# Kernel tuning notes

Measured on AMD Instinct MI355X. Metric: run time of the kernel, lower is better.

Reference implementation:

```python
import jax, jax.numpy as jnp
import numpy as np

ATTN, ENC, DEC = 1024, 1024, 1024
B, S = 64, 2048

def setup_inputs() -> dict:
    key = jax.random.key(0)
    k1, k2, k3, k4, k5, k6 = jax.random.split(key, 6)
    sc_w = 1.0 / np.sqrt(ENC + DEC)
    sc_v = 1.0 / np.sqrt(ATTN)
    return {
        "hidden": jax.random.normal(k1, (B, DEC), dtype=jnp.float32),
        "vectors_to_attend": jax.random.normal(k2, (S, B, ENC), dtype=jnp.float32),
        "attn_w_weight": jax.random.uniform(k3, (ATTN, ENC + DEC), jnp.float32, -sc_w, sc_w),
        "attn_w_bias": jax.random.uniform(k4, (ATTN,), jnp.float32, -sc_w, sc_w),
        "attn_v_weight": jax.random.uniform(k5, (1, ATTN), jnp.float32, -sc_v, sc_v),
        "attn_v_bias": jax.random.uniform(k6, (1,), jnp.float32, -sc_v, sc_v),
    }

def reference(hidden, vectors_to_attend, attn_w_weight, attn_w_bias, attn_v_weight, attn_v_bias):
    # vectors_to_attend: [S, B, E] -> [B, S, E]
    v = jnp.transpose(vectors_to_attend, (1, 0, 2))
    # Split attn_w over the concat dim: concat([v, h]) @ W^T == v @ We^T + h @ Wd^T
    We = attn_w_weight[:, :ENC]   # [A, E]
    Wd = attn_w_weight[:, ENC:]   # [A, D]
    # energies: [B, S, A]
    e = jnp.tanh(jnp.einsum('bse,ae->bsa', v, We)
                 + jnp.einsum('bd,ad->ba', hidden, Wd)[:, None, :]
                 + attn_w_bias)
    # scores: [B, S]
    scores = jnp.einsum('bsa,a->bs', e, attn_v_weight[0]) + attn_v_bias[0]
    weights = jax.nn.softmax(scores, axis=1)          # softmax over seq dim
    context = jnp.einsum('bs,bse->be', weights, v)    # [B, E]
    return context[:, None, :]                        # [B, 1, E] to match bmm output
```

## Files before the change

kernel.cpp:

```cpp
#include <hip/hip_runtime.h>
#include <hip/hip_bf16.h>
#include <math.h>

#define BB 64
#define SS 2048
#define MT (SS*BB)
#define NT 16

typedef __attribute__((ext_vector_type(4))) float f4;
typedef __attribute__((ext_vector_type(8))) short s8;

__device__ __forceinline__ unsigned short f2bf(float x) {
  union { float f; unsigned u; } v; v.f = x;
  unsigned r = v.u + 0x7FFFu + ((v.u >> 16) & 1u);
  return (unsigned short)(r >> 16);
}
__device__ __forceinline__ float bf2f(unsigned short x) {
  union { unsigned u; float f; } v; v.u = ((unsigned)x) << 16;
  return v.f;
}
__device__ __forceinline__ float fast_tanh(float x) {
  float t = __expf(2.0f * x);
  return 1.0f - 2.0f * __builtin_amdgcn_rcpf(t + 1.0f);
}

#define GLD16(gp, lp) __builtin_amdgcn_global_load_lds( \
    (const __attribute__((address_space(1))) void*)(gp), \
    (__attribute__((address_space(3))) void*)(lp), 16, 0, 0)
#define WAITV4() asm volatile("s_waitcnt vmcnt(4)" ::: "memory")
#define WAITV0() asm volatile("s_waitcnt vmcnt(0)" ::: "memory")
#define BAR()    __builtin_amdgcn_s_barrier()
#define SCHED0() __builtin_amdgcn_sched_barrier(0)

__global__ void k_pack(const float* __restrict__ src, unsigned short* __restrict__ dst,
                       int stride) {
  __shared__ float ls[64][260];
  int g = blockIdx.x, cb = blockIdx.y, tid = threadIdx.x;
  int cl = (tid & 63) * 4, rbk = tid >> 6;
  const float* s0 = src + (size_t)(g * 64) * stride + cb * 256 + cl;
  #pragma unroll
  for (int it = 0; it < 16; ++it) {
    int rr = it * 4 + rbk;
    *(f4*)&ls[rr][cl] = *(const f4*)(s0 + (size_t)rr * stride);
  }
  __syncthreads();
  int kt_l = tid >> 6;
  int rr = tid & 63;
  int kt = cb * 4 + kt_l;
  int grow = g * 64 + rr;
  int panel = grow >> 8, pr = grow & 255, h = pr >> 7, r = pr & 127;
  unsigned short* d = dst + (((size_t)panel * 16 + kt) * 2 + h) * 8192 + r * 64;
  int rx = r & 7;
  #pragma unroll
  for (int sp = 0; sp < 8; ++sp) {
    const float* q = &ls[rr][kt_l * 64 + ((sp ^ rx) * 8)];
    f4 x0 = *(const f4*)q, x1 = *(const f4*)(q + 4);
    s8 o;
    #pragma unroll
    for (int j = 0; j < 4; ++j) { o[j] = (short)f2bf(x0[j]); o[4 + j] = (short)f2bf(x1[j]); }
    *(s8*)(d + sp * 8) = o;
  }
}

__global__ void k_hp(const float* __restrict__ hidden, const float* __restrict__ w,
                     const float* __restrict__ wbias, float* __restrict__ hp) {
  __shared__ float hs[1024];
  int b = blockIdx.x, tid = threadIdx.x;
  for (int i = tid; i < 1024; i += 256) hs[i] = hidden[b * 1024 + i];
  __syncthreads();
  int a = blockIdx.y * 256 + tid;
  const f4* wd = (const f4*)(w + a * 2048 + 1024);
  const f4* hv = (const f4*)hs;
  float acc = wbias[a];
  #pragma unroll 8
  for (int d = 0; d < 256; ++d) {
    f4 x = wd[d], y = hv[d];
    acc += x[0]*y[0] + x[1]*y[1] + x[2]*y[2] + x[3]*y[3];
  }
  hp[b * 1024 + a] = acc;
}

__global__ __launch_bounds__(512, 1) void k_gemm(
    const unsigned short* __restrict__ Avbs, const unsigned short* __restrict__ Wbs,
    const float* __restrict__ hp, const float* __restrict__ vw,
    float* __restrict__ part, int bm0, int nbm) {
  extern __shared__ char smem[];
  int bid = blockIdx.x;
  int nwg = nbm * 4;
  int wg = bid;
  if ((nwg & 7) == 0) { int cpx = nwg >> 3; wg = (bid & 7) * cpx + (bid >> 3); }
  int bn = wg & 3;
  int bmL = wg >> 2;
  int tid = threadIdx.x, lane = tid & 63;
  int wid = tid >> 6, wr = wid >> 2, wc = wid & 3;
  int c = lane & 15, kq = lane >> 4;

  int sx0 = ((kq) ^ (c & 7)) << 4;
  int sx1 = ((4 + kq) ^ (c & 7)) << 4;
  int aoff = wr * 16384 + c * 128;
  int boff = 32768 + (wc >> 1) * 16384 + ((wc & 1) * 64 + c) * 128;

  const unsigned short* Abase = Avbs + (size_t)bmL * 262144 + tid * 8;
  const unsigned short* Bbase = Wbs + (size_t)bn * 262144 + tid * 8;
  auto stage = [&](int tt, int u) {
    char* d = smem + (tt & 1) * 65536 + u * 16384 + tid * 16;
    const unsigned short* s = ((u & 2) ? Bbase : Abase) + ((size_t)tt * 2 + (u & 1)) * 8192;
    GLD16(s, d);
    GLD16(s + 4096, d + 8192);
  };

  f4 acc[8][4];
  f4 z = {0.f, 0.f, 0.f, 0.f};
  #pragma unroll
  for (int i = 0; i < 8; ++i)
    #pragma unroll
    for (int j = 0; j < 4; ++j) acc[i][j] = z;

  s8 vaC[4], vaN[4], vb0[4], vb1[4];

#define LDSA(DST, BASE, SX) { const char* p_ = (BASE) + (SX); \
    DST[0] = *(const s8*)(p_);        DST[1] = *(const s8*)(p_ + 2048); \
    DST[2] = *(const s8*)(p_ + 4096); DST[3] = *(const s8*)(p_ + 6144); }
#define LDB(RB, DST, SX) { const char* bb_ = (RB) + boff + (SX); \
    DST[0] = *(const s8*)(bb_);        DST[1] = *(const s8*)(bb_ + 2048); \
    DST[2] = *(const s8*)(bb_ + 4096); DST[3] = *(const s8*)(bb_ + 6144); }
#define MM(mh, VA, VB) { \
    __builtin_amdgcn_s_setprio(1); \
    _Pragma("unroll") \
    for (int m_ = 0; m_ < 4; ++m_) { \
      acc[(mh)*4+m_][0] = __builtin_amdgcn_mfma_f32_16x16x32_bf16(VA[m_], VB[0], acc[(mh)*4+m_][0], 0, 0, 0); \
      acc[(mh)*4+m_][1] = __builtin_amdgcn_mfma_f32_16x16x32_bf16(VA[m_], VB[1], acc[(mh)*4+m_][1], 0, 0, 0); \
      acc[(mh)*4+m_][2] = __builtin_amdgcn_mfma_f32_16x16x32_bf16(VA[m_], VB[2], acc[(mh)*4+m_][2], 0, 0, 0); \
      acc[(mh)*4+m_][3] = __builtin_amdgcn_mfma_f32_16x16x32_bf16(VA[m_], VB[3], acc[(mh)*4+m_][3], 0, 0, 0); \
    } \
    __builtin_amdgcn_s_setprio(0); }

  stage(0, 0); stage(0, 1); stage(0, 2); stage(0, 3);
  stage(1, 2); stage(1, 3);
  WAITV4();
  BAR();
  SCHED0();
  {
    const char* rb = smem;
    LDSA(vaC, rb + aoff, sx0);
    LDB(rb, vb0, sx0);
  }

  #pragma unroll 1
  for (int t = 0; t < NT; ++t) {
    const char* rb = smem + (t & 1) * 65536;
    const char* ab = rb + aoff;
    if (t < 15) stage(t + 1, 0);
    MM(0, vaC, vb0);
    LDSA(vaN, ab, sx1);
    LDB(rb, vb1, sx1);
    if (t < 15) stage(t + 1, 1);
    MM(0, vaN, vb1);
    LDSA(vaC, ab + 8192, sx0);
    SCHED0();
    BAR();
    SCHED0();
    if (t < 14) stage(t + 2, 2);
    MM(1, vaC, vb0);
    LDSA(vaN, ab + 8192, sx1);
    if (t < 14) stage(t + 2, 3);
    MM(1, vaN, vb1);
    if (t < 15) {
      if (t < 14) WAITV4(); else WAITV0();
      SCHED0();
      BAR();
      SCHED0();
      const char* nrb = smem + ((t + 1) & 1) * 65536;
      LDSA(vaC, nrb + aoff, sx0);
      LDB(nrb, vb0, sx0);
    }
  }
#undef LDSA
#undef LDB
#undef MM

  __syncthreads();
  {
    const float* hprow = hp + bn * 256;
    float* lhp = (float*)smem;
    #pragma unroll
    for (int qd = 0; qd < 8; ++qd) {
      int i = qd * 512 + tid;
      int b = i >> 6, col4 = i & 63;
      *(f4*)(lhp + b * 256 + col4 * 4) = *(const f4*)(hprow + (size_t)b * 1024 + col4 * 4);
    }
  }
  __syncthreads();
  const float* lhpf = (const float*)smem;

  int lg = kq;
  int bm = bm0 + bmL;
  float rs[8][4];
  #pragma unroll
  for (int mi = 0; mi < 8; ++mi)
    #pragma unroll
    for (int j = 0; j < 4; ++j) rs[mi][j] = 0.f;
  #pragma unroll
  for (int ni = 0; ni < 4; ++ni) {
    int colL = wc * 64 + ni * 16 + c;
    float vwa = vw[bn * 256 + colL];
    #pragma unroll
    for (int mi = 0; mi < 8; ++mi) {
      #pragma unroll
      for (int j = 0; j < 4; ++j) {
        int r = wr * 128 + mi * 16 + lg * 4 + j;
        int b = r & 63;
        float x = acc[mi][ni][j] + lhpf[b * 256 + colL];
        rs[mi][j] += fast_tanh(x) * vwa;
      }
    }
  }
  #pragma unroll
  for (int off = 1; off < 16; off <<= 1) {
    #pragma unroll
    for (int mi = 0; mi < 8; ++mi)
      #pragma unroll
      for (int j = 0; j < 4; ++j)
        rs[mi][j] += __shfl_xor(rs[mi][j], off, 64);
  }
  if (c == 0) {
    int p = bn * 4 + wc;
    #pragma unroll
    for (int mi = 0; mi < 8; ++mi)
      #pragma unroll
      for (int j = 0; j < 4; ++j) {
        int m = bm * 256 + wr * 128 + mi * 16 + lg * 4 + j;
        int b = m & 63, s = m >> 6;
        part[(size_t)p * MT + b * SS + s] = rs[mi][j];
      }
  }
}

__global__ void k_softmax(const float* __restrict__ part, float* __restrict__ wt) {
  int b = blockIdx.x, tid = threadIdx.x, lane = tid & 63, wid = tid >> 6;
  __shared__ float red[8];
  float sc[8];
  float mx = -1e30f;
  #pragma unroll
  for (int i = 0; i < 8; ++i) {
    int s = tid + i * 256;
    float a = 0.f;
    #pragma unroll
    for (int p = 0; p < 16; ++p) a += part[(size_t)p * MT + b * SS + s];
    sc[i] = a; mx = fmaxf(mx, a);
  }
  for (int o = 1; o < 64; o <<= 1) mx = fmaxf(mx, __shfl_xor(mx, o, 64));
  if (lane == 0) red[wid] = mx;
  __syncthreads();
  mx = fmaxf(fmaxf(red[0], red[1]), fmaxf(red[2], red[3]));
  float sum = 0.f;
  #pragma unroll
  for (int i = 0; i < 8; ++i) { sc[i] = expf(sc[i] - mx); sum += sc[i]; }
  for (int o = 1; o < 64; o <<= 1) sum += __shfl_xor(sum, o, 64);
  if (lane == 0) red[4 + wid] = sum;
  __syncthreads();
  sum = red[4] + red[5] + red[6] + red[7];
  float inv = 1.f / sum;
  #pragma unroll
  for (int i = 0; i < 8; ++i) wt[b * SS + tid + i * 256] = sc[i] * inv;
}

__global__ void k_ctx_bfs(const unsigned short* __restrict__ vbs, const float* __restrict__ wt,
                          float* __restrict__ ctxp) {
  int b = blockIdx.x, cch = blockIdx.y, tid = threadIdx.x;
  int e = tid * 4;
  int kt = e >> 6, sl = (e >> 3) & 7, off = e & 7;
  f4 acc = {0.f, 0.f, 0.f, 0.f};
  int s0 = cch * 128;
  const float* wrow = wt + b * SS;
  #pragma unroll 4
  for (int s = s0; s < s0 + 128; ++s) {
    float ws = wrow[s];
    int row = s * 64 + b;
    int panel = row >> 8, pr = row & 255, h = pr >> 7, r = pr & 127;
    size_t addr = (((size_t)panel * 16 + kt) * 2 + h) * 8192 + r * 64 + ((sl ^ (r & 7)) << 3) + off;
    ushort4 u = *(const ushort4*)(vbs + addr);
    acc[0] += bf2f(u.x) * ws;
    acc[1] += bf2f(u.y) * ws;
    acc[2] += bf2f(u.z) * ws;
    acc[3] += bf2f(u.w) * ws;
  }
  *(f4*)(ctxp + (size_t)(cch * 64 + b) * 1024 + tid * 4) = acc;
}

__global__ void k_ctx_f32(const float* __restrict__ v, const float* __restrict__ wt,
                          float* __restrict__ ctxp) {
  int b = blockIdx.x, cch = blockIdx.y, tid = threadIdx.x;
  f4 acc = {0.f, 0.f, 0.f, 0.f};
  int s0 = cch * 128;
  const float* wrow = wt + b * SS;
  #pragma unroll 4
  for (int s = s0; s < s0 + 128; ++s) {
    float ws = wrow[s];
    const f4* vp = (const f4*)(v + (size_t)(s * 64 + b) * 1024);
    acc += vp[tid] * ws;
  }
  *(f4*)(ctxp + (size_t)(cch * 64 + b) * 1024 + tid * 4) = acc;
}

__global__ void k_out(const float* __restrict__ ctxp, float* __restrict__ out) {
  int b = blockIdx.x, tid = threadIdx.x;
  f4 acc = {0.f, 0.f, 0.f, 0.f};
  #pragma unroll
  for (int cch = 0; cch < 16; ++cch)
    acc += *(const f4*)(ctxp + (size_t)(cch * 64 + b) * 1024 + tid * 4);
  *(f4*)(out + b * 1024 + tid * 4) = acc;
}

extern "C" void kernel_launch(void* const* d_in, const int* in_sizes, int n_in,
                              void* d_out, int out_size, void* d_ws, size_t ws_size,
                              hipStream_t stream) {
  const float* hidden = (const float*)d_in[0];
  const float* v      = (const float*)d_in[1];
  const float* ww     = (const float*)d_in[2];
  const float* wbias  = (const float*)d_in[3];
  const float* vwgt   = (const float*)d_in[4];
  float* out = (float*)d_out;

  char* ws = (char*)d_ws;
  float*          hp   = (float*)(ws);
  unsigned short* wbs  = (unsigned short*)(ws + 262144);
  float*          part = (float*)(ws + 262144 + 2097152);
  float*          wt   = (float*)(ws + 262144 + 2097152 + 8388608);
  float*          ctxp = (float*)(ws + 262144 + 2097152 + 8388608 + 524288);
  size_t fixed = 262144 + 2097152 + 8388608 + 524288 + 4194304;
  unsigned short* vbs  = (unsigned short*)(ws + fixed);

  size_t avail = (ws_size > fixed) ? (ws_size - fixed) : 0;
  long rows_chunk = (long)(avail / 2048) & ~511L;
  if (rows_chunk > MT) rows_chunk = MT;
  if (rows_chunk < 512) rows_chunk = 512;
  int nchunks = (int)((MT + rows_chunk - 1) / rows_chunk);

  hipFuncSetAttribute((const void*)k_gemm, hipFuncAttributeMaxDynamicSharedMemorySize, 131072);

  k_pack<<<dim3(16, 4), 256, 0, stream>>>(ww, wbs, 2048);
  k_hp<<<dim3(64, 4), 256, 0, stream>>>(hidden, ww, wbias, hp);

  for (long r0 = 0; r0 < MT; r0 += rows_chunk) {
    long nr = MT - r0; if (nr > rows_chunk) nr = rows_chunk;
    int nbm = (int)(nr / 256);
    k_pack<<<dim3((int)(nr / 64), 4), 256, 0, stream>>>(v + (size_t)r0 * 1024, vbs, 1024);
    k_gemm<<<nbm * 4, 512, 131072, stream>>>(vbs, wbs, hp, vwgt, part, (int)(r0 / 256), nbm);
  }

  k_softmax<<<64, 256, 0, stream>>>(part, wt);
  if (nchunks == 1)
    k_ctx_bfs<<<dim3(64, 16), 256, 0, stream>>>(vbs, wt, ctxp);
  else
    k_ctx_f32<<<dim3(64, 16), 256, 0, stream>>>(v, wt, ctxp);
  k_out<<<64, 256, 0, stream>>>(ctxp, out);
}
```

Before: 576.4 us.

## Quantize energy GEMM operands to FP8 and use scaled f8f6f4 MFMA

The packing kernel now converts the attended vectors and the attention weight to FP8 instead of bf16. The GEMM uses the 16x16x128 scaled f8f6f4 MFMA with unit scales, which halves the K iterations and halves the bytes packed and staged through LDS. Because the packed FP8 copy is too lossy for the context sum, the context kernel always reads the original fp32 vectors. This trades extra fp32 traffic in that pass, and accuracy of the energies and softmax scores, for lower GEMM compute and memory traffic.

```diff
diff --git a/kernel.cpp b/kernel.cpp
--- a/kernel.cpp
+++ b/kernel.cpp
@@ -5,20 +5,12 @@
 #define BB 64
 #define SS 2048
 #define MT (SS*BB)
-#define NT 16
+#define NT 8
 
 typedef __attribute__((ext_vector_type(4))) float f4;
-typedef __attribute__((ext_vector_type(8))) short s8;
-
-__device__ __forceinline__ unsigned short f2bf(float x) {
-  union { float f; unsigned u; } v; v.f = x;
-  unsigned r = v.u + 0x7FFFu + ((v.u >> 16) & 1u);
-  return (unsigned short)(r >> 16);
-}
-__device__ __forceinline__ float bf2f(unsigned short x) {
-  union { unsigned u; float f; } v; v.u = ((unsigned)x) << 16;
-  return v.f;
-}
+typedef __attribute__((ext_vector_type(4))) int   i4;
+typedef __attribute__((ext_vector_type(8))) int   i8;
+
 __device__ __forceinline__ float fast_tanh(float x) {
   float t = __expf(2.0f * x);
   return 1.0f - 2.0f * __builtin_amdgcn_rcpf(t + 1.0f);
@@ -32,8 +24,8 @@
 #define BAR()    __builtin_amdgcn_s_barrier()
 #define SCHED0() __builtin_amdgcn_sched_barrier(0)
 
-__global__ void k_pack(const float* __restrict__ src, unsigned short* __restrict__ dst,
-                       int stride) {
+__global__ void k_packq(const float* __restrict__ src, unsigned char* __restrict__ dst,
+                        int stride) {
   __shared__ float ls[64][260];
   int g = blockIdx.x, cb = blockIdx.y, tid = threadIdx.x;
   int cl = (tid & 63) * 4, rbk = tid >> 6;
@@ -44,21 +36,27 @@
     *(f4*)&ls[rr][cl] = *(const f4*)(s0 + (size_t)rr * stride);
   }
   __syncthreads();
-  int kt_l = tid >> 6;
   int rr = tid & 63;
-  int kt = cb * 4 + kt_l;
+  int q = tid >> 6;
+  int kt = cb * 2 + (q >> 1);
   int grow = g * 64 + rr;
   int panel = grow >> 8, pr = grow & 255, h = pr >> 7, r = pr & 127;
-  unsigned short* d = dst + (((size_t)panel * 16 + kt) * 2 + h) * 8192 + r * 64;
   int rx = r & 7;
-  #pragma unroll
-  for (int sp = 0; sp < 8; ++sp) {
-    const float* q = &ls[rr][kt_l * 64 + ((sp ^ rx) * 8)];
-    f4 x0 = *(const f4*)q, x1 = *(const f4*)(q + 4);
-    s8 o;
-    #pragma unroll
-    for (int j = 0; j < 4; ++j) { o[j] = (short)f2bf(x0[j]); o[4 + j] = (short)f2bf(x1[j]); }
-    *(s8*)(d + sp * 8) = o;
+  unsigned char* ub = dst + (((size_t)(panel * 8 + kt) * 2 + h) * 128 + r) * 128;
+  #pragma unroll
+  for (int si = 0; si < 4; ++si) {
+    int s = (q & 1) * 4 + si;
+    int sp = s ^ rx;
+    const float* fp = &ls[rr][q * 64 + si * 16];
+    i4 w;
+    #pragma unroll
+    for (int k = 0; k < 4; ++k) {
+      int b = 0;
+      b = __builtin_amdgcn_cvt_pk_fp8_f32(fp[k * 4 + 0], fp[k * 4 + 1], b, 0);
+      b = __builtin_amdgcn_cvt_pk_fp8_f32(fp[k * 4 + 2], fp[k * 4 + 3], b, 1);
+      w[k] = b;
+    }
+    *(i4*)(ub + sp * 16) = w;
   }
 }
 
@@ -80,8 +78,15 @@
   hp[b * 1024 + a] = acc;
 }
 
+__device__ __forceinline__ i8 build8(i4 lo, i4 hi) {
+  i8 r;
+  r[0] = lo[0]; r[1] = lo[1]; r[2] = lo[2]; r[3] = lo[3];
+  r[4] = hi[0]; r[5] = hi[1]; r[6] = hi[2]; r[7] = hi[3];
+  return r;
+}
+
 __global__ __launch_bounds__(512, 1) void k_gemm(
-    const unsigned short* __restrict__ Avbs, const unsigned short* __restrict__ Wbs,
+    const unsigned char* __restrict__ Aq, const unsigned char* __restrict__ Wq,
     const float* __restrict__ hp, const float* __restrict__ vw,
     float* __restrict__ part, int bm0, int nbm) {
   extern __shared__ char smem[];
@@ -95,18 +100,18 @@
   int wid = tid >> 6, wr = wid >> 2, wc = wid & 3;
   int c = lane & 15, kq = lane >> 4;
 
-  int sx0 = ((kq) ^ (c & 7)) << 4;
-  int sx1 = ((4 + kq) ^ (c & 7)) << 4;
-  int aoff = wr * 16384 + c * 128;
-  int boff = 32768 + (wc >> 1) * 16384 + ((wc & 1) * 64 + c) * 128;
-
-  const unsigned short* Abase = Avbs + (size_t)bmL * 262144 + tid * 8;
-  const unsigned short* Bbase = Wbs + (size_t)bn * 262144 + tid * 8;
+  int sx0 = ((2 * kq) ^ (c & 7)) << 4;
+  int sx1 = sx0 ^ 16;
+  int aoff0 = wr * 16384 + c * 128;
+  int boff0 = 32768 + (wc >> 1) * 16384 + ((wc & 1) * 64 + c) * 128;
+
+  const unsigned char* Abase = Aq + (size_t)bmL * 262144 + tid * 16;
+  const unsigned char* Bbase = Wq + (size_t)bn * 262144 + tid * 16;
   auto stage = [&](int tt, int u) {
     char* d = smem + (tt & 1) * 65536 + u * 16384 + tid * 16;
-    const unsigned short* s = ((u & 2) ? Bbase : Abase) + ((size_t)tt * 2 + (u & 1)) * 8192;
+    const unsigned char* s = ((u & 2) ? Bbase : Abase) + ((size_t)tt * 2 + (u & 1)) * 16384;
     GLD16(s, d);
-    GLD16(s + 4096, d + 8192);
+    GLD16(s + 8192, d + 8192);
   };
 
   f4 acc[8][4];
@@ -116,22 +121,28 @@
     #pragma unroll
     for (int j = 0; j < 4; ++j) acc[i][j] = z;
 
-  s8 vaC[4], vaN[4], vb0[4], vb1[4];
-
-#define LDSA(DST, BASE, SX) { const char* p_ = (BASE) + (SX); \
-    DST[0] = *(const s8*)(p_);        DST[1] = *(const s8*)(p_ + 2048); \
-    DST[2] = *(const s8*)(p_ + 4096); DST[3] = *(const s8*)(p_ + 6144); }
-#define LDB(RB, DST, SX) { const char* bb_ = (RB) + boff + (SX); \
-    DST[0] = *(const s8*)(bb_);        DST[1] = *(const s8*)(bb_ + 2048); \
-    DST[2] = *(const s8*)(bb_ + 4096); DST[3] = *(const s8*)(bb_ + 6144); }
-#define MM(mh, VA, VB) { \
+  i8 a03[4], a47[4], bfr[4];
+
+#define LD_A(DST, RB, MI0) { const char* p_ = (RB) + aoff0; \
+    _Pragma("unroll") \
+    for (int m_ = 0; m_ < 4; ++m_) { \
+      i4 lo_ = *(const i4*)(p_ + ((MI0) + m_) * 2048 + sx0); \
+      i4 hi_ = *(const i4*)(p_ + ((MI0) + m_) * 2048 + sx1); \
+      DST[m_] = build8(lo_, hi_); } }
+#define LD_B(DST, RB) { const char* p_ = (RB) + boff0; \
+    _Pragma("unroll") \
+    for (int n_ = 0; n_ < 4; ++n_) { \
+      i4 lo_ = *(const i4*)(p_ + n_ * 2048 + sx0); \
+      i4 hi_ = *(const i4*)(p_ + n_ * 2048 + sx1); \
+      DST[n_] = build8(lo_, hi_); } }
+#define MM(MB, VA, VB) { \
     __builtin_amdgcn_s_setprio(1); \
     _Pragma("unroll") \
     for (int m_ = 0; m_ < 4; ++m_) { \
-      acc[(mh)*4+m_][0] = __builtin_amdgcn_mfma_f32_16x16x32_bf16(VA[m_], VB[0], acc[(mh)*4+m_][0], 0, 0, 0); \
-      acc[(mh)*4+m_][1] = __builtin_amdgcn_mfma_f32_16x16x32_bf16(VA[m_], VB[1], acc[(mh)*4+m_][1], 0, 0, 0); \
-      acc[(mh)*4+m_][2] = __builtin_amdgcn_mfma_f32_16x16x32_bf16(VA[m_], VB[2], acc[(mh)*4+m_][2], 0, 0, 0); \
-      acc[(mh)*4+m_][3] = __builtin_amdgcn_mfma_f32_16x16x32_bf16(VA[m_], VB[3], acc[(mh)*4+m_][3], 0, 0, 0); \
+      acc[(MB)+m_][0] = __builtin_amdgcn_mfma_scale_f32_16x16x128_f8f6f4(VA[m_], VB[0], acc[(MB)+m_][0], 0, 0, 0, 0x7F7F7F7F, 0, 0x7F7F7F7F); \
+      acc[(MB)+m_][1] = __builtin_amdgcn_mfma_scale_f32_16x16x128_f8f6f4(VA[m_], VB[1], acc[(MB)+m_][1], 0, 0, 0, 0x7F7F7F7F, 0, 0x7F7F7F7F); \
+      acc[(MB)+m_][2] = __builtin_amdgcn_mfma_scale_f32_16x16x128_f8f6f4(VA[m_], VB[2], acc[(MB)+m_][2], 0, 0, 0, 0x7F7F7F7F, 0, 0x7F7F7F7F); \
+      acc[(MB)+m_][3] = __builtin_amdgcn_mfma_scale_f32_16x16x128_f8f6f4(VA[m_], VB[3], acc[(MB)+m_][3], 0, 0, 0, 0x7F7F7F7F, 0, 0x7F7F7F7F); \
     } \
     __builtin_amdgcn_s_setprio(0); }
 
@@ -140,43 +151,32 @@
   WAITV4();
   BAR();
   SCHED0();
-  {
-    const char* rb = smem;
-    LDSA(vaC, rb + aoff, sx0);
-    LDB(rb, vb0, sx0);
-  }
+  LD_A(a03, smem, 0);
+  LD_B(bfr, smem);
 
   #pragma unroll 1
   for (int t = 0; t < NT; ++t) {
     const char* rb = smem + (t & 1) * 65536;
-    const char* ab = rb + aoff;
-    if (t < 15) stage(t + 1, 0);
-    MM(0, vaC, vb0);
-    LDSA(vaN, ab, sx1);
-    LDB(rb, vb1, sx1);
-    if (t < 15) stage(t + 1, 1);
-    MM(0, vaN, vb1);
-    LDSA(vaC, ab + 8192, sx0);
+    if (t < 7) { stage(t + 1, 0); stage(t + 1, 1); }
+    MM(0, a03, bfr);
+    LD_A(a47, rb, 4);
     SCHED0();
     BAR();
     SCHED0();
-    if (t < 14) stage(t + 2, 2);
-    MM(1, vaC, vb0);
-    LDSA(vaN, ab + 8192, sx1);
-    if (t < 14) stage(t + 2, 3);
-    MM(1, vaN, vb1);
-    if (t < 15) {
-      if (t < 14) WAITV4(); else WAITV0();
+    if (t < 6) { stage(t + 2, 2); stage(t + 2, 3); }
+    MM(4, a47, bfr);
+    if (t < 7) {
+      if (t < 6) WAITV4(); else WAITV0();
       SCHED0();
       BAR();
       SCHED0();
-      const char* nrb = smem + ((t + 1) & 1) * 65536;
-      LDSA(vaC, nrb + aoff, sx0);
-      LDB(nrb, vb0, sx0);
+      const char* nb = smem + ((t + 1) & 1) * 65536;
+      LD_A(a03, nb, 0);
+      LD_B(bfr, nb);
     }
   }
-#undef LDSA
-#undef LDB
+#undef LD_A
+#undef LD_B
 #undef MM
 
   __syncthreads();
@@ -263,29 +263,6 @@
   float inv = 1.f / sum;
   #pragma unroll
   for (int i = 0; i < 8; ++i) wt[b * SS + tid + i * 256] = sc[i] * inv;
-}
-
-__global__ void k_ctx_bfs(const unsigned short* __restrict__ vbs, const float* __restrict__ wt,
-                          float* __restrict__ ctxp) {
-  int b = blockIdx.x, cch = blockIdx.y, tid = threadIdx.x;
-  int e = tid * 4;
-  int kt = e >> 6, sl = (e >> 3) & 7, off = e & 7;
-  f4 acc = {0.f, 0.f, 0.f, 0.f};
-  int s0 = cch * 128;
-  const float* wrow = wt + b * SS;
-  #pragma unroll 4
-  for (int s = s0; s < s0 + 128; ++s) {
-    float ws = wrow[s];
-    int row = s * 64 + b;
-    int panel = row >> 8, pr = row & 255, h = pr >> 7, r = pr & 127;
-    size_t addr = (((size_t)panel * 16 + kt) * 2 + h) * 8192 + r * 64 + ((sl ^ (r & 7)) << 3) + off;
-    ushort4 u = *(const ushort4*)(vbs + addr);
-    acc[0] += bf2f(u.x) * ws;
-    acc[1] += bf2f(u.y) * ws;
-    acc[2] += bf2f(u.z) * ws;
-    acc[3] += bf2f(u.w) * ws;
-  }
-  *(f4*)(ctxp + (size_t)(cch * 64 + b) * 1024 + tid * 4) = acc;
 }
 
 __global__ void k_ctx_f32(const float* __restrict__ v, const float* __restrict__ wt,
@@ -324,35 +301,31 @@
 
   char* ws = (char*)d_ws;
   float*          hp   = (float*)(ws);
-  unsigned short* wbs  = (unsigned short*)(ws + 262144);
-  float*          part = (float*)(ws + 262144 + 2097152);
-  float*          wt   = (float*)(ws + 262144 + 2097152 + 8388608);
-  float*          ctxp = (float*)(ws + 262144 + 2097152 + 8388608 + 524288);
-  size_t fixed = 262144 + 2097152 + 8388608 + 524288 + 4194304;
-  unsigned short* vbs  = (unsigned short*)(ws + fixed);
+  unsigned char*  wq   = (unsigned char*)(ws + 262144);
+  float*          part = (float*)(ws + 262144 + 1048576);
+  float*          wt   = (float*)(ws + 262144 + 1048576 + 8388608);
+  float*          ctxp = (float*)(ws + 262144 + 1048576 + 8388608 + 524288);
+  size_t fixed = 262144 + 1048576 + 8388608 + 524288 + 4194304;
+  unsigned char*  vq   = (unsigned char*)(ws + fixed);
 
   size_t avail = (ws_size > fixed) ? (ws_size - fixed) : 0;
-  long rows_chunk = (long)(avail / 2048) & ~511L;
+  long rows_chunk = (long)(avail / 1024) & ~511L;
   if (rows_chunk > MT) rows_chunk = MT;
   if (rows_chunk < 512) rows_chunk = 512;
-  int nchunks = (int)((MT + rows_chunk - 1) / rows_chunk);
 
   hipFuncSetAttribute((const void*)k_gemm, hipFuncAttributeMaxDynamicSharedMemorySize, 131072);
 
-  k_pack<<<dim3(16, 4), 256, 0, stream>>>(ww, wbs, 2048);
+  k_packq<<<dim3(16, 4), 256, 0, stream>>>(ww, wq, 2048);
   k_hp<<<dim3(64, 4), 256, 0, stream>>>(hidden, ww, wbias, hp);
 
   for (long r0 = 0; r0 < MT; r0 += rows_chunk) {
     long nr = MT - r0; if (nr > rows_chunk) nr = rows_chunk;
     int nbm = (int)(nr / 256);
-    k_pack<<<dim3((int)(nr / 64), 4), 256, 0, stream>>>(v + (size_t)r0 * 1024, vbs, 1024);
-    k_gemm<<<nbm * 4, 512, 131072, stream>>>(vbs, wbs, hp, vwgt, part, (int)(r0 / 256), nbm);
+    k_packq<<<dim3((int)(nr / 64), 4), 256, 0, stream>>>(v + (size_t)r0 * 1024, vq, 1024);
+    k_gemm<<<nbm * 4, 512, 131072, stream>>>(vq, wq, hp, vwgt, part, (int)(r0 / 256), nbm);
   }
 
   k_softmax<<<64, 256, 0, stream>>>(part, wt);
-  if (nchunks == 1)
-    k_ctx_bfs<<<dim3(64, 16), 256, 0, stream>>>(vbs, wt, ctxp);
-  else
-    k_ctx_f32<<<dim3(64, 16), 256, 0, stream>>>(v, wt, ctxp);
+  k_ctx_f32<<<dim3(64, 16), 256, 0, stream>>>(v, wt, ctxp);
   k_out<<<64, 256, 0, stream>>>(ctxp, out);
 }
```

New measurement: 878.6 us. +52.4%, slower.
